# Performance work log

Hardware: AMD Instinct MI355X
Metric: run time of the kernel (lower is better)

## Reference

```python
import jax, jax.numpy as jnp
import numpy as np

B, H, SQ, SKV, D, TOPK = 1, 16, 1024, 4096, 128, 64


def setup_inputs() -> dict:
    key = jax.random.key(0)
    kq, kk, kv, ki, ks = jax.random.split(key, 5)
    q = jax.random.normal(kq, (B, H, SQ, D), dtype=jnp.float32)
    k = jax.random.normal(kk, (B, H, SKV, D), dtype=jnp.float32)
    v = jax.random.normal(kv, (B, H, SKV, D), dtype=jnp.float32)
    topk_indices = jax.random.randint(ki, (B, SQ, TOPK), 0, SKV, dtype=jnp.int32)
    topk_scores = jax.random.uniform(ks, (B, SQ, TOPK), dtype=jnp.float32)
    return {"q": q, "k": k, "v": v, "topk_indices": topk_indices,
            "topk_scores": topk_scores}


def reference(q, k, v, topk_indices, topk_scores):
    # q: (b,h,s,d); k,v: (b,h,S,d) global (cp_world_size=1 all-gather is identity)
    head_dim = q.shape[-1]
    scale = head_dim ** -0.5
    # Gather selected K/V per query without dense (b,h,s,S,d) expansion.
    # idx: (b,1,s,topk,1) broadcast against (b,h,1,S,d) along axis=3.
    idx = topk_indices[:, None, :, :, None]
    k_g = jnp.take_along_axis(k[:, :, None, :, :], idx, axis=3)  # (b,h,s,t,d)
    v_g = jnp.take_along_axis(v[:, :, None, :, :], idx, axis=3)  # (b,h,s,t,d)
    scores = jnp.einsum("bhsd,bhstd->bhst", q, k_g) * scale
    w = jax.nn.softmax(scores, axis=-1)
    # rescale by indexer scores and renormalize
    w = w * topk_scores[:, None, :, :]
    w = w / (jnp.sum(w, axis=-1, keepdims=True) + 1e-12)
    out = jnp.einsum("bhst,bhstd->bhsd", w, v_g)
    return out
```

## Files before the change

kernel.cpp:

```cpp
#include <hip/hip_runtime.h>
#include <hip/hip_fp16.h>

#define NH  16
#define SQL 1024
#define SKV 4096
#define HD  128
#define TK  64

typedef _Float16 h2_t __attribute__((ext_vector_type(2)));
typedef float    f32x4 __attribute__((ext_vector_type(4)));

__device__ __forceinline__ unsigned pkh(float x, float y) {
    return (unsigned)__half_as_ushort(__float2half(x)) |
           ((unsigned)__half_as_ushort(__float2half(y)) << 16);
}

__global__ __launch_bounds__(256) void cvt_f16(
    const float* __restrict__ k, const float* __restrict__ v,
    unsigned short* __restrict__ kh, unsigned short* __restrict__ vh)
{
    int b = blockIdx.x;
    const float* src; unsigned short* dst;
    if (b < 4096) { src = k; dst = kh; }
    else          { src = v; dst = vh; b -= 4096; }
    const size_t i = (size_t)b * 256 + threadIdx.x;
    const float4* s4 = (const float4*)src;
    float4 a = s4[2 * i], c = s4[2 * i + 1];
    uint4 o;
    o.x = pkh(a.x, a.y);
    o.y = pkh(a.z, a.w);
    o.z = pkh(c.x, c.y);
    o.w = pkh(c.z, c.w);
    ((uint4*)dst)[i] = o;
}

__global__ __launch_bounds__(256, 2) void dsa_phased(
    const float* __restrict__ q, const unsigned short* __restrict__ kh,
    const unsigned short* __restrict__ vh, const int* __restrict__ tidx,
    const float* __restrict__ tsc, float* __restrict__ out)
{
    __shared__ float scr[4][TK][17];

    const int tid  = threadIdx.x;
    const int wv   = tid >> 6;
    const int lane = tid & 63;
    const int quad = lane >> 4;
    const int l16  = lane & 15;
    const int bi   = blockIdx.x;
    const int xcd  = bi & 7;
    const int tile = bi >> 3;
    const int sb   = tile * 16 + wv * 4;

    int   tIdx[4];
    float tSc[4];
#pragma unroll
    for (int qi = 0; qi < 4; ++qi) {
        tIdx[qi] = tidx[(sb + qi) * TK + lane];
        tSc[qi]  = tsc[(sb + qi) * TK + lane];
    }

    for (int rnd = 0; rnd < 2; ++rnd) {
        const int h = xcd | (rnd << 3);
        const unsigned short* kb = kh + (size_t)h * SKV * HD;
        const unsigned short* vb = vh + (size_t)h * SKV * HD;
        unsigned wpk[4];

#pragma unroll
        for (int qi = 0; qi < 4; ++qi) {
            const int s = sb + qi;
            const float* qp = q + (size_t)(h * SQL + s) * HD + 8 * l16;
            const f32x4 qa = __builtin_nontemporal_load((const f32x4*)qp);
            const f32x4 qb = __builtin_nontemporal_load((const f32x4*)qp + 1);
            h2_t q0 = {(_Float16)qa.x, (_Float16)qa.y};
            h2_t q1 = {(_Float16)qa.z, (_Float16)qa.w};
            h2_t q2 = {(_Float16)qb.x, (_Float16)qb.y};
            h2_t q3 = {(_Float16)qb.z, (_Float16)qb.w};

            float part[16];
#pragma unroll
            for (int i = 0; i < 16; ++i) {
                const size_t row = (size_t)__shfl(tIdx[qi], 4 * i + quad);
                uint4 kw = *(const uint4*)(kb + row * HD + 8 * l16);
                float d = 0.f;
#if __has_builtin(__builtin_amdgcn_fdot2)
                d = __builtin_amdgcn_fdot2(q0, __builtin_bit_cast(h2_t, kw.x), d, false);
                d = __builtin_amdgcn_fdot2(q1, __builtin_bit_cast(h2_t, kw.y), d, false);
                d = __builtin_amdgcn_fdot2(q2, __builtin_bit_cast(h2_t, kw.z), d, false);
                d = __builtin_amdgcn_fdot2(q3, __builtin_bit_cast(h2_t, kw.w), d, false);
#else
                {
                    float2 k0 = __half22float2(__builtin_bit_cast(__half2, kw.x));
                    float2 k1 = __half22float2(__builtin_bit_cast(__half2, kw.y));
                    float2 k2 = __half22float2(__builtin_bit_cast(__half2, kw.z));
                    float2 k3 = __half22float2(__builtin_bit_cast(__half2, kw.w));
                    d  = qa.x * k0.x + qa.y * k0.y + qa.z * k1.x + qa.w * k1.y;
                    d += qb.x * k2.x + qb.y * k2.y + qb.z * k3.x + qb.w * k3.y;
                }
#endif
                part[i] = d;
            }

#pragma unroll
            for (int i = 0; i < 16; ++i) scr[wv][4 * i + quad][l16] = part[i];
            float acc = 0.f;
#pragma unroll
            for (int m = 0; m < 16; ++m) acc += scr[wv][lane][m];
            acc *= 0.08838834764831845f;

            float mx = acc;
#pragma unroll
            for (int off = 32; off; off >>= 1) mx = fmaxf(mx, __shfl_xor(mx, off));
            const float e   = __expf(acc - mx);
            const float ets = e * tSc[qi];
            float se = e, sets = ets;
#pragma unroll
            for (int off = 32; off; off >>= 1) {
                se   += __shfl_xor(se, off);
                sets += __shfl_xor(sets, off);
            }
            const float w = ets / (sets + 1e-12f * se);
            wpk[qi] = __builtin_bit_cast(unsigned, __float2half2_rn(w));
        }

        __syncthreads();

#pragma unroll
        for (int qi = 0; qi < 4; ++qi) {
            const int s = sb + qi;
            __half2 o0 = __float2half2_rn(0.f);
            __half2 o1 = o0, o2 = o0, o3 = o0;
#pragma unroll
            for (int i = 0; i < 16; ++i) {
                const size_t row = (size_t)__shfl(tIdx[qi], 4 * i + quad);
                uint4 vw = *(const uint4*)(vb + row * HD + 8 * l16);
                const __half2 w2 =
                    __builtin_bit_cast(__half2, __shfl(wpk[qi], 4 * i + quad));
                o0 = __hfma2(w2, __builtin_bit_cast(__half2, vw.x), o0);
                o1 = __hfma2(w2, __builtin_bit_cast(__half2, vw.y), o1);
                o2 = __hfma2(w2, __builtin_bit_cast(__half2, vw.z), o2);
                o3 = __hfma2(w2, __builtin_bit_cast(__half2, vw.w), o3);
            }

            __half2 oo[4] = {o0, o1, o2, o3};
#pragma unroll
            for (int j = 0; j < 4; ++j) {
                unsigned u = __builtin_bit_cast(unsigned, oo[j]);
                oo[j] = __hadd2(oo[j], __builtin_bit_cast(__half2, __shfl_xor(u, 16)));
                u = __builtin_bit_cast(unsigned, oo[j]);
                oo[j] = __hadd2(oo[j], __builtin_bit_cast(__half2, __shfl_xor(u, 32)));
            }

            if (quad == 0) {
                float2 f0 = __half22float2(oo[0]);
                float2 f1 = __half22float2(oo[1]);
                float2 f2 = __half22float2(oo[2]);
                float2 f3 = __half22float2(oo[3]);
                float* op = out + (size_t)(h * SQL + s) * HD + 8 * l16;
                f32x4 w0 = {f0.x, f0.y, f1.x, f1.y};
                f32x4 w1 = {f2.x, f2.y, f3.x, f3.y};
                __builtin_nontemporal_store(w0, (f32x4*)op);
                __builtin_nontemporal_store(w1, (f32x4*)op + 1);
            }
        }
        if (rnd == 0) __syncthreads();
    }
}

__global__ __launch_bounds__(256) void dsa_fp32(
    const float* __restrict__ q, const float* __restrict__ k,
    const float* __restrict__ v, const int* __restrict__ tidx,
    const float* __restrict__ tsc, float* __restrict__ out)
{
    __shared__ int   idxs[4][TK];
    __shared__ float wsc[4][TK];
    const int tid = threadIdx.x, wv = tid >> 6, lane = tid & 63;
    const int half = lane >> 5, l32 = lane & 31, bi = blockIdx.x;
    const int h = ((bi & 7) << 1) | ((bi >> 3) & 1);
    const int s = ((bi >> 4) << 2) + wv;
    const float* qp = q + (size_t)(h * SQL + s) * HD;
    const float4 qf = *(const float4*)(qp + 4 * l32);
    const float t_sc = tsc[s * TK + lane];
    idxs[wv][lane] = tidx[s * TK + lane];
    const float* kb = k + (size_t)h * SKV * HD;
#pragma unroll 4
    for (int i = 0; i < TK / 2; ++i) {
        const int t = 2 * i + half, row = idxs[wv][t];
        float4 k4 = *(const float4*)(kb + (size_t)row * HD + 4 * l32);
        float d = k4.x * qf.x + k4.y * qf.y + k4.z * qf.z + k4.w * qf.w;
        d += __shfl_xor(d, 16); d += __shfl_xor(d, 8); d += __shfl_xor(d, 4);
        d += __shfl_xor(d, 2);  d += __shfl_xor(d, 1);
        if (l32 == 0) wsc[wv][t] = d;
    }
    float acc = wsc[wv][lane] * 0.08838834764831845f;
    float m = acc;
#pragma unroll
    for (int off = 32; off; off >>= 1) m = fmaxf(m, __shfl_xor(m, off));
    const float e = __expf(acc - m), ets = e * t_sc;
    float se = e, sets = ets;
#pragma unroll
    for (int off = 32; off; off >>= 1) { se += __shfl_xor(se, off); sets += __shfl_xor(sets, off); }
    wsc[wv][lane] = ets / (sets + 1e-12f * se);
    const float* vbp = v + (size_t)h * SKV * HD;
    float4 o = make_float4(0.f, 0.f, 0.f, 0.f);
#pragma unroll 4
    for (int i = 0; i < TK / 2; ++i) {
        const int t = 2 * i + half, row = idxs[wv][t];
        const float wt = wsc[wv][t];
        float4 v4 = *(const float4*)(vbp + (size_t)row * HD + 4 * l32);
        o.x += wt * v4.x; o.y += wt * v4.y; o.z += wt * v4.z; o.w += wt * v4.w;
    }
    o.x += __shfl_xor(o.x, 32); o.y += __shfl_xor(o.y, 32);
    o.z += __shfl_xor(o.z, 32); o.w += __shfl_xor(o.w, 32);
    if (half == 0) *(float4*)(out + (size_t)(h * SQL + s) * HD + 4 * l32) = o;
}

extern "C" void kernel_launch(void* const* d_in, const int* in_sizes, int n_in,
                              void* d_out, int out_size, void* d_ws, size_t ws_size,
                              hipStream_t stream) {
    const float* q  = (const float*)d_in[0];
    const float* k  = (const float*)d_in[1];
    const float* v  = (const float*)d_in[2];
    const int*   ti = (const int*)d_in[3];
    const float* ts = (const float*)d_in[4];
    float* out = (float*)d_out;

    const size_t nkv  = (size_t)NH * SKV * HD;
    const size_t need = 2 * nkv * sizeof(unsigned short);
    if (ws_size >= need) {
        unsigned short* kh = (unsigned short*)d_ws;
        unsigned short* vh = kh + nkv;
        cvt_f16<<<dim3(8192), dim3(256), 0, stream>>>(k, v, kh, vh);
        dsa_phased<<<dim3(512), dim3(256), 0, stream>>>(q, kh, vh, ti, ts, out);
    } else {
        dsa_fp32<<<dim3(4096), dim3(256), 0, stream>>>(q, k, v, ti, ts, out);
    }
}
```

Baseline: 133.5 us.

## Drop fp16 K/V conversion pass and gather fp32 K/V directly

Removes the separate kernel that converted all of K and V to fp16 in a workspace, and has the attention kernel gather fp32 K/V rows directly, using fp32 FMAs for the dot products and the weighted V sum. The fp16 pass read and wrote all 64 MB of K/V even though the top-64 gather touches only part of it, so skipping it avoids that full-tensor traffic and one kernel launch. Each wave now handles two queries instead of four, and the grid doubles to 1024 blocks to keep the GPU busy. In exchange each gathered row is twice as many bytes, and the fp32 fallback path is deleted.

```diff
diff --git a/kernel.cpp b/kernel.cpp
--- a/kernel.cpp
+++ b/kernel.cpp
@@ -1,5 +1,4 @@
 #include <hip/hip_runtime.h>
-#include <hip/hip_fp16.h>
 
 #define NH  16
 #define SQL 1024
@@ -7,36 +6,11 @@
 #define HD  128
 #define TK  64
 
-typedef _Float16 h2_t __attribute__((ext_vector_type(2)));
-typedef float    f32x4 __attribute__((ext_vector_type(4)));
+typedef float f32x4 __attribute__((ext_vector_type(4)));
 
-__device__ __forceinline__ unsigned pkh(float x, float y) {
-    return (unsigned)__half_as_ushort(__float2half(x)) |
-           ((unsigned)__half_as_ushort(__float2half(y)) << 16);
-}
-
-__global__ __launch_bounds__(256) void cvt_f16(
-    const float* __restrict__ k, const float* __restrict__ v,
-    unsigned short* __restrict__ kh, unsigned short* __restrict__ vh)
-{
-    int b = blockIdx.x;
-    const float* src; unsigned short* dst;
-    if (b < 4096) { src = k; dst = kh; }
-    else          { src = v; dst = vh; b -= 4096; }
-    const size_t i = (size_t)b * 256 + threadIdx.x;
-    const float4* s4 = (const float4*)src;
-    float4 a = s4[2 * i], c = s4[2 * i + 1];
-    uint4 o;
-    o.x = pkh(a.x, a.y);
-    o.y = pkh(a.z, a.w);
-    o.z = pkh(c.x, c.y);
-    o.w = pkh(c.z, c.w);
-    ((uint4*)dst)[i] = o;
-}
-
-__global__ __launch_bounds__(256, 2) void dsa_phased(
-    const float* __restrict__ q, const unsigned short* __restrict__ kh,
-    const unsigned short* __restrict__ vh, const int* __restrict__ tidx,
+__global__ __launch_bounds__(256) void dsa_direct(
+    const float* __restrict__ q, const float* __restrict__ k,
+    const float* __restrict__ v, const int* __restrict__ tidx,
     const float* __restrict__ tsc, float* __restrict__ out)
 {
     __shared__ float scr[4][TK][17];
@@ -49,54 +23,44 @@
     const int bi   = blockIdx.x;
     const int xcd  = bi & 7;
     const int tile = bi >> 3;
-    const int sb   = tile * 16 + wv * 4;
+    const int sb   = tile * 8 + wv * 2;
 
-    int   tIdx[4];
-    float tSc[4];
+    int   tIdx[2];
+    float tSc[2];
 #pragma unroll
-    for (int qi = 0; qi < 4; ++qi) {
+    for (int qi = 0; qi < 2; ++qi) {
         tIdx[qi] = tidx[(sb + qi) * TK + lane];
         tSc[qi]  = tsc[(sb + qi) * TK + lane];
     }
 
     for (int rnd = 0; rnd < 2; ++rnd) {
         const int h = xcd | (rnd << 3);
-        const unsigned short* kb = kh + (size_t)h * SKV * HD;
-        const unsigned short* vb = vh + (size_t)h * SKV * HD;
-        unsigned wpk[4];
+        const float* kb = k + (size_t)h * SKV * HD;
+        const float* vb = v + (size_t)h * SKV * HD;
+        float wq[2];
 
 #pragma unroll
-        for (int qi = 0; qi < 4; ++qi) {
+        for (int qi = 0; qi < 2; ++qi) {
             const int s = sb + qi;
             const float* qp = q + (size_t)(h * SQL + s) * HD + 8 * l16;
             const f32x4 qa = __builtin_nontemporal_load((const f32x4*)qp);
             const f32x4 qb = __builtin_nontemporal_load((const f32x4*)qp + 1);
-            h2_t q0 = {(_Float16)qa.x, (_Float16)qa.y};
-            h2_t q1 = {(_Float16)qa.z, (_Float16)qa.w};
-            h2_t q2 = {(_Float16)qb.x, (_Float16)qb.y};
-            h2_t q3 = {(_Float16)qb.z, (_Float16)qb.w};
 
             float part[16];
 #pragma unroll
             for (int i = 0; i < 16; ++i) {
                 const size_t row = (size_t)__shfl(tIdx[qi], 4 * i + quad);
-                uint4 kw = *(const uint4*)(kb + row * HD + 8 * l16);
-                float d = 0.f;
-#if __has_builtin(__builtin_amdgcn_fdot2)
-                d = __builtin_amdgcn_fdot2(q0, __builtin_bit_cast(h2_t, kw.x), d, false);
-                d = __builtin_amdgcn_fdot2(q1, __builtin_bit_cast(h2_t, kw.y), d, false);
-                d = __builtin_amdgcn_fdot2(q2, __builtin_bit_cast(h2_t, kw.z), d, false);
-                d = __builtin_amdgcn_fdot2(q3, __builtin_bit_cast(h2_t, kw.w), d, false);
-#else
-                {
-                    float2 k0 = __half22float2(__builtin_bit_cast(__half2, kw.x));
-                    float2 k1 = __half22float2(__builtin_bit_cast(__half2, kw.y));
-                    float2 k2 = __half22float2(__builtin_bit_cast(__half2, kw.z));
-                    float2 k3 = __half22float2(__builtin_bit_cast(__half2, kw.w));
-                    d  = qa.x * k0.x + qa.y * k0.y + qa.z * k1.x + qa.w * k1.y;
-                    d += qb.x * k2.x + qb.y * k2.y + qb.z * k3.x + qb.w * k3.y;
-                }
-#endif
+                const f32x4 ka = *(const f32x4*)(kb + row * HD + 8 * l16);
+                const f32x4 kc = *(const f32x4*)(kb + row * HD + 8 * l16 + 4);
+                float d;
+                d = qa.x * ka.x;
+                d = fmaf(qa.y, ka.y, d);
+                d = fmaf(qa.z, ka.z, d);
+                d = fmaf(qa.w, ka.w, d);
+                d = fmaf(qb.x, kc.x, d);
+                d = fmaf(qb.y, kc.y, d);
+                d = fmaf(qb.z, kc.z, d);
+                d = fmaf(qb.w, kc.w, d);
                 part[i] = d;
             }
 
@@ -118,100 +82,49 @@
                 se   += __shfl_xor(se, off);
                 sets += __shfl_xor(sets, off);
             }
-            const float w = ets / (sets + 1e-12f * se);
-            wpk[qi] = __builtin_bit_cast(unsigned, __float2half2_rn(w));
+            wq[qi] = ets / (sets + 1e-12f * se);
         }
 
         __syncthreads();
 
 #pragma unroll
-        for (int qi = 0; qi < 4; ++qi) {
+        for (int qi = 0; qi < 2; ++qi) {
             const int s = sb + qi;
-            __half2 o0 = __float2half2_rn(0.f);
-            __half2 o1 = o0, o2 = o0, o3 = o0;
+            float o0 = 0.f, o1 = 0.f, o2 = 0.f, o3 = 0.f;
+            float o4 = 0.f, o5 = 0.f, o6 = 0.f, o7 = 0.f;
 #pragma unroll
             for (int i = 0; i < 16; ++i) {
                 const size_t row = (size_t)__shfl(tIdx[qi], 4 * i + quad);
-                uint4 vw = *(const uint4*)(vb + row * HD + 8 * l16);
-                const __half2 w2 =
-                    __builtin_bit_cast(__half2, __shfl(wpk[qi], 4 * i + quad));
-                o0 = __hfma2(w2, __builtin_bit_cast(__half2, vw.x), o0);
-                o1 = __hfma2(w2, __builtin_bit_cast(__half2, vw.y), o1);
-                o2 = __hfma2(w2, __builtin_bit_cast(__half2, vw.z), o2);
-                o3 = __hfma2(w2, __builtin_bit_cast(__half2, vw.w), o3);
+                const f32x4 va = *(const f32x4*)(vb + row * HD + 8 * l16);
+                const f32x4 vc = *(const f32x4*)(vb + row * HD + 8 * l16 + 4);
+                const float wt = __shfl(wq[qi], 4 * i + quad);
+                o0 = fmaf(wt, va.x, o0);
+                o1 = fmaf(wt, va.y, o1);
+                o2 = fmaf(wt, va.z, o2);
+                o3 = fmaf(wt, va.w, o3);
+                o4 = fmaf(wt, vc.x, o4);
+                o5 = fmaf(wt, vc.y, o5);
+                o6 = fmaf(wt, vc.z, o6);
+                o7 = fmaf(wt, vc.w, o7);
             }
 
-            __half2 oo[4] = {o0, o1, o2, o3};
+            float oo[8] = {o0, o1, o2, o3, o4, o5, o6, o7};
 #pragma unroll
-            for (int j = 0; j < 4; ++j) {
-                unsigned u = __builtin_bit_cast(unsigned, oo[j]);
-                oo[j] = __hadd2(oo[j], __builtin_bit_cast(__half2, __shfl_xor(u, 16)));
-                u = __builtin_bit_cast(unsigned, oo[j]);
-                oo[j] = __hadd2(oo[j], __builtin_bit_cast(__half2, __shfl_xor(u, 32)));
+            for (int j = 0; j < 8; ++j) {
+                oo[j] += __shfl_xor(oo[j], 16);
+                oo[j] += __shfl_xor(oo[j], 32);
             }
 
             if (quad == 0) {
-                float2 f0 = __half22float2(oo[0]);
-                float2 f1 = __half22float2(oo[1]);
-                float2 f2 = __half22float2(oo[2]);
-                float2 f3 = __half22float2(oo[3]);
                 float* op = out + (size_t)(h * SQL + s) * HD + 8 * l16;
-                f32x4 w0 = {f0.x, f0.y, f1.x, f1.y};
-                f32x4 w1 = {f2.x, f2.y, f3.x, f3.y};
+                f32x4 w0 = {oo[0], oo[1], oo[2], oo[3]};
+                f32x4 w1 = {oo[4], oo[5], oo[6], oo[7]};
                 __builtin_nontemporal_store(w0, (f32x4*)op);
                 __builtin_nontemporal_store(w1, (f32x4*)op + 1);
             }
         }
         if (rnd == 0) __syncthreads();
     }
-}
-
-__global__ __launch_bounds__(256) void dsa_fp32(
-    const float* __restrict__ q, const float* __restrict__ k,
-    const float* __restrict__ v, const int* __restrict__ tidx,
-    const float* __restrict__ tsc, float* __restrict__ out)
-{
-    __shared__ int   idxs[4][TK];
-    __shared__ float wsc[4][TK];
-    const int tid = threadIdx.x, wv = tid >> 6, lane = tid & 63;
-    const int half = lane >> 5, l32 = lane & 31, bi = blockIdx.x;
-    const int h = ((bi & 7) << 1) | ((bi >> 3) & 1);
-    const int s = ((bi >> 4) << 2) + wv;
-    const float* qp = q + (size_t)(h * SQL + s) * HD;
-    const float4 qf = *(const float4*)(qp + 4 * l32);
-    const float t_sc = tsc[s * TK + lane];
-    idxs[wv][lane] = tidx[s * TK + lane];
-    const float* kb = k + (size_t)h * SKV * HD;
-#pragma unroll 4
-    for (int i = 0; i < TK / 2; ++i) {
-        const int t = 2 * i + half, row = idxs[wv][t];
-        float4 k4 = *(const float4*)(kb + (size_t)row * HD + 4 * l32);
-        float d = k4.x * qf.x + k4.y * qf.y + k4.z * qf.z + k4.w * qf.w;
-        d += __shfl_xor(d, 16); d += __shfl_xor(d, 8); d += __shfl_xor(d, 4);
-        d += __shfl_xor(d, 2);  d += __shfl_xor(d, 1);
-        if (l32 == 0) wsc[wv][t] = d;
-    }
-    float acc = wsc[wv][lane] * 0.08838834764831845f;
-    float m = acc;
-#pragma unroll
-    for (int off = 32; off; off >>= 1) m = fmaxf(m, __shfl_xor(m, off));
-    const float e = __expf(acc - m), ets = e * t_sc;
-    float se = e, sets = ets;
-#pragma unroll
-    for (int off = 32; off; off >>= 1) { se += __shfl_xor(se, off); sets += __shfl_xor(sets, off); }
-    wsc[wv][lane] = ets / (sets + 1e-12f * se);
-    const float* vbp = v + (size_t)h * SKV * HD;
-    float4 o = make_float4(0.f, 0.f, 0.f, 0.f);
-#pragma unroll 4
-    for (int i = 0; i < TK / 2; ++i) {
-        const int t = 2 * i + half, row = idxs[wv][t];
-        const float wt = wsc[wv][t];
-        float4 v4 = *(const float4*)(vbp + (size_t)row * HD + 4 * l32);
-        o.x += wt * v4.x; o.y += wt * v4.y; o.z += wt * v4.z; o.w += wt * v4.w;
-    }
-    o.x += __shfl_xor(o.x, 32); o.y += __shfl_xor(o.y, 32);
-    o.z += __shfl_xor(o.z, 32); o.w += __shfl_xor(o.w, 32);
-    if (half == 0) *(float4*)(out + (size_t)(h * SQL + s) * HD + 4 * l32) = o;
 }
 
 extern "C" void kernel_launch(void* const* d_in, const int* in_sizes, int n_in,
@@ -224,14 +137,6 @@
     const float* ts = (const float*)d_in[4];
     float* out = (float*)d_out;
 
-    const size_t nkv  = (size_t)NH * SKV * HD;
-    const size_t need = 2 * nkv * sizeof(unsigned short);
-    if (ws_size >= need) {
-        unsigned short* kh = (unsigned short*)d_ws;
-        unsigned short* vh = kh + nkv;
-        cvt_f16<<<dim3(8192), dim3(256), 0, stream>>>(k, v, kh, vh);
-        dsa_phased<<<dim3(512), dim3(256), 0, stream>>>(q, kh, vh, ti, ts, out);
-    } else {
-        dsa_fp32<<<dim3(4096), dim3(256), 0, stream>>>(q, k, v, ti, ts, out);
-    }
+    (void)d_ws; (void)ws_size;
+    dsa_direct<<<dim3(1024), dim3(256), 0, stream>>>(q, k, v, ti, ts, out);
 }
```

New measurement: 166.3 us. 24.6% more time.

## Align f16 conversion with XCD head mapping and use one query per wave

Applied to the files above, without the earlier changes.

The K/V fp32-to-f16 conversion kernel now assigns blocks so each XCD converts the heads that the same XCD later gathers in the attention kernel, aiming for L2 locality between kernels. The attention kernel is restructured so each wave processes a single query rather than four, quadrupling the grid and reducing per-thread register state. This trades some redundant per-block setup for more parallelism and latency hiding.

```diff
diff --git a/kernel.cpp b/kernel.cpp
--- a/kernel.cpp
+++ b/kernel.cpp
@@ -7,7 +7,7 @@
 #define HD  128
 #define TK  64
 
-typedef _Float16 h2_t __attribute__((ext_vector_type(2)));
+typedef _Float16 h2_t  __attribute__((ext_vector_type(2)));
 typedef float    f32x4 __attribute__((ext_vector_type(4)));
 
 __device__ __forceinline__ unsigned pkh(float x, float y) {
@@ -15,26 +15,37 @@
            ((unsigned)__half_as_ushort(__float2half(y)) << 16);
 }
 
-__global__ __launch_bounds__(256) void cvt_f16(
+__global__ __launch_bounds__(256) void cvt_f16_xcd(
     const float* __restrict__ k, const float* __restrict__ v,
     unsigned short* __restrict__ kh, unsigned short* __restrict__ vh)
 {
-    int b = blockIdx.x;
-    const float* src; unsigned short* dst;
-    if (b < 4096) { src = k; dst = kh; }
-    else          { src = v; dst = vh; b -= 4096; }
-    const size_t i = (size_t)b * 256 + threadIdx.x;
-    const float4* s4 = (const float4*)src;
-    float4 a = s4[2 * i], c = s4[2 * i + 1];
-    uint4 o;
-    o.x = pkh(a.x, a.y);
-    o.y = pkh(a.z, a.w);
-    o.z = pkh(c.x, c.y);
-    o.w = pkh(c.z, c.w);
-    ((uint4*)dst)[i] = o;
-}
-
-__global__ __launch_bounds__(256, 2) void dsa_phased(
+    const int b   = blockIdx.x;
+    const int xcd = b & 7;
+    const int j   = b >> 3;
+    const int isK = j >> 8;
+    const int hsel= (j >> 7) & 1;
+    const int chk = j & 127;
+    const int h   = xcd | (hsel << 3);
+
+    const float*    src = isK ? k  : v;
+    unsigned short* dst = isK ? kh : vh;
+    const size_t base = (size_t)h * SKV * HD + (size_t)chk * 4096
+                      + (size_t)threadIdx.x * 16;
+    const float4* s4 = (const float4*)(src + base);
+    uint4*        d4 = (uint4*)(dst + base);
+#pragma unroll
+    for (int u = 0; u < 2; ++u) {
+        float4 a = s4[2 * u], c = s4[2 * u + 1];
+        uint4 o;
+        o.x = pkh(a.x, a.y);
+        o.y = pkh(a.z, a.w);
+        o.z = pkh(c.x, c.y);
+        o.w = pkh(c.z, c.w);
+        d4[u] = o;
+    }
+}
+
+__global__ __launch_bounds__(256) void dsa_f16p(
     const float* __restrict__ q, const unsigned short* __restrict__ kh,
     const unsigned short* __restrict__ vh, const int* __restrict__ tidx,
     const float* __restrict__ tsc, float* __restrict__ out)
@@ -48,120 +59,105 @@
     const int l16  = lane & 15;
     const int bi   = blockIdx.x;
     const int xcd  = bi & 7;
-    const int tile = bi >> 3;
-    const int sb   = tile * 16 + wv * 4;
-
-    int   tIdx[4];
-    float tSc[4];
-#pragma unroll
-    for (int qi = 0; qi < 4; ++qi) {
-        tIdx[qi] = tidx[(sb + qi) * TK + lane];
-        tSc[qi]  = tsc[(sb + qi) * TK + lane];
-    }
+    const int s0   = (bi >> 3) * 4 + wv;
+
+    const int   tIdx = tidx[s0 * TK + lane];
+    const float tSc  = tsc[s0 * TK + lane];
 
     for (int rnd = 0; rnd < 2; ++rnd) {
         const int h = xcd | (rnd << 3);
         const unsigned short* kb = kh + (size_t)h * SKV * HD;
         const unsigned short* vb = vh + (size_t)h * SKV * HD;
-        unsigned wpk[4];
-
-#pragma unroll
-        for (int qi = 0; qi < 4; ++qi) {
-            const int s = sb + qi;
-            const float* qp = q + (size_t)(h * SQL + s) * HD + 8 * l16;
-            const f32x4 qa = __builtin_nontemporal_load((const f32x4*)qp);
-            const f32x4 qb = __builtin_nontemporal_load((const f32x4*)qp + 1);
-            h2_t q0 = {(_Float16)qa.x, (_Float16)qa.y};
-            h2_t q1 = {(_Float16)qa.z, (_Float16)qa.w};
-            h2_t q2 = {(_Float16)qb.x, (_Float16)qb.y};
-            h2_t q3 = {(_Float16)qb.z, (_Float16)qb.w};
-
-            float part[16];
-#pragma unroll
-            for (int i = 0; i < 16; ++i) {
-                const size_t row = (size_t)__shfl(tIdx[qi], 4 * i + quad);
-                uint4 kw = *(const uint4*)(kb + row * HD + 8 * l16);
-                float d = 0.f;
+
+        const float* qp = q + (size_t)(h * SQL + s0) * HD + 8 * l16;
+        const f32x4 qa = __builtin_nontemporal_load((const f32x4*)qp);
+        const f32x4 qb = __builtin_nontemporal_load((const f32x4*)qp + 1);
+        h2_t q0 = {(_Float16)qa.x, (_Float16)qa.y};
+        h2_t q1 = {(_Float16)qa.z, (_Float16)qa.w};
+        h2_t q2 = {(_Float16)qb.x, (_Float16)qb.y};
+        h2_t q3 = {(_Float16)qb.z, (_Float16)qb.w};
+
+        float part[16];
+#pragma unroll
+        for (int i = 0; i < 16; ++i) {
+            const size_t row = (size_t)__shfl(tIdx, 4 * i + quad);
+            uint4 kw = *(const uint4*)(kb + row * HD + 8 * l16);
+            float d = 0.f;
 #if __has_builtin(__builtin_amdgcn_fdot2)
-                d = __builtin_amdgcn_fdot2(q0, __builtin_bit_cast(h2_t, kw.x), d, false);
-                d = __builtin_amdgcn_fdot2(q1, __builtin_bit_cast(h2_t, kw.y), d, false);
-                d = __builtin_amdgcn_fdot2(q2, __builtin_bit_cast(h2_t, kw.z), d, false);
-                d = __builtin_amdgcn_fdot2(q3, __builtin_bit_cast(h2_t, kw.w), d, false);
+            d = __builtin_amdgcn_fdot2(q0, __builtin_bit_cast(h2_t, kw.x), d, false);
+            d = __builtin_amdgcn_fdot2(q1, __builtin_bit_cast(h2_t, kw.y), d, false);
+            d = __builtin_amdgcn_fdot2(q2, __builtin_bit_cast(h2_t, kw.z), d, false);
+            d = __builtin_amdgcn_fdot2(q3, __builtin_bit_cast(h2_t, kw.w), d, false);
 #else
-                {
-                    float2 k0 = __half22float2(__builtin_bit_cast(__half2, kw.x));
-                    float2 k1 = __half22float2(__builtin_bit_cast(__half2, kw.y));
-                    float2 k2 = __half22float2(__builtin_bit_cast(__half2, kw.z));
-                    float2 k3 = __half22float2(__builtin_bit_cast(__half2, kw.w));
-                    d  = qa.x * k0.x + qa.y * k0.y + qa.z * k1.x + qa.w * k1.y;
-                    d += qb.x * k2.x + qb.y * k2.y + qb.z * k3.x + qb.w * k3.y;
-                }
+            {
+                float2 k0 = __half22float2(__builtin_bit_cast(__half2, kw.x));
+                float2 k1 = __half22float2(__builtin_bit_cast(__half2, kw.y));
+                float2 k2 = __half22float2(__builtin_bit_cast(__half2, kw.z));
+                float2 k3 = __half22float2(__builtin_bit_cast(__half2, kw.w));
+                d  = qa.x * k0.x + qa.y * k0.y + qa.z * k1.x + qa.w * k1.y;
+                d += qb.x * k2.x + qb.y * k2.y + qb.z * k3.x + qb.w * k3.y;
+            }
 #endif
-                part[i] = d;
-            }
-
-#pragma unroll
-            for (int i = 0; i < 16; ++i) scr[wv][4 * i + quad][l16] = part[i];
-            float acc = 0.f;
-#pragma unroll
-            for (int m = 0; m < 16; ++m) acc += scr[wv][lane][m];
-            acc *= 0.08838834764831845f;
-
-            float mx = acc;
-#pragma unroll
-            for (int off = 32; off; off >>= 1) mx = fmaxf(mx, __shfl_xor(mx, off));
-            const float e   = __expf(acc - mx);
-            const float ets = e * tSc[qi];
-            float se = e, sets = ets;
-#pragma unroll
-            for (int off = 32; off; off >>= 1) {
-                se   += __shfl_xor(se, off);
-                sets += __shfl_xor(sets, off);
-            }
-            const float w = ets / (sets + 1e-12f * se);
-            wpk[qi] = __builtin_bit_cast(unsigned, __float2half2_rn(w));
-        }
+            part[i] = d;
+        }
+
+#pragma unroll
+        for (int i = 0; i < 16; ++i) scr[wv][4 * i + quad][l16] = part[i];
+        float acc = 0.f;
+#pragma unroll
+        for (int m = 0; m < 16; ++m) acc += scr[wv][lane][m];
+        acc *= 0.08838834764831845f;
+
+        float mx = acc;
+#pragma unroll
+        for (int off = 32; off; off >>= 1) mx = fmaxf(mx, __shfl_xor(mx, off));
+        const float e   = __expf(acc - mx);
+        const float ets = e * tSc;
+        float se = e, sets = ets;
+#pragma unroll
+        for (int off = 32; off; off >>= 1) {
+            se   += __shfl_xor(se, off);
+            sets += __shfl_xor(sets, off);
+        }
+        const float w = ets / (sets + 1e-12f * se);
+        const unsigned wpk = __builtin_bit_cast(unsigned, __float2half2_rn(w));
 
         __syncthreads();
 
-#pragma unroll
-        for (int qi = 0; qi < 4; ++qi) {
-            const int s = sb + qi;
-            __half2 o0 = __float2half2_rn(0.f);
-            __half2 o1 = o0, o2 = o0, o3 = o0;
-#pragma unroll
-            for (int i = 0; i < 16; ++i) {
-                const size_t row = (size_t)__shfl(tIdx[qi], 4 * i + quad);
-                uint4 vw = *(const uint4*)(vb + row * HD + 8 * l16);
-                const __half2 w2 =
-                    __builtin_bit_cast(__half2, __shfl(wpk[qi], 4 * i + quad));
-                o0 = __hfma2(w2, __builtin_bit_cast(__half2, vw.x), o0);
-                o1 = __hfma2(w2, __builtin_bit_cast(__half2, vw.y), o1);
-                o2 = __hfma2(w2, __builtin_bit_cast(__half2, vw.z), o2);
-                o3 = __hfma2(w2, __builtin_bit_cast(__half2, vw.w), o3);
-            }
-
-            __half2 oo[4] = {o0, o1, o2, o3};
-#pragma unroll
-            for (int j = 0; j < 4; ++j) {
-                unsigned u = __builtin_bit_cast(unsigned, oo[j]);
-                oo[j] = __hadd2(oo[j], __builtin_bit_cast(__half2, __shfl_xor(u, 16)));
-                u = __builtin_bit_cast(unsigned, oo[j]);
-                oo[j] = __hadd2(oo[j], __builtin_bit_cast(__half2, __shfl_xor(u, 32)));
-            }
-
-            if (quad == 0) {
-                float2 f0 = __half22float2(oo[0]);
-                float2 f1 = __half22float2(oo[1]);
-                float2 f2 = __half22float2(oo[2]);
-                float2 f3 = __half22float2(oo[3]);
-                float* op = out + (size_t)(h * SQL + s) * HD + 8 * l16;
-                f32x4 w0 = {f0.x, f0.y, f1.x, f1.y};
-                f32x4 w1 = {f2.x, f2.y, f3.x, f3.y};
-                __builtin_nontemporal_store(w0, (f32x4*)op);
-                __builtin_nontemporal_store(w1, (f32x4*)op + 1);
-            }
-        }
+        __half2 o0 = __float2half2_rn(0.f);
+        __half2 o1 = o0, o2 = o0, o3 = o0;
+#pragma unroll
+        for (int i = 0; i < 16; ++i) {
+            const size_t row = (size_t)__shfl(tIdx, 4 * i + quad);
+            uint4 vw = *(const uint4*)(vb + row * HD + 8 * l16);
+            const __half2 w2 = __builtin_bit_cast(__half2, __shfl(wpk, 4 * i + quad));
+            o0 = __hfma2(w2, __builtin_bit_cast(__half2, vw.x), o0);
+            o1 = __hfma2(w2, __builtin_bit_cast(__half2, vw.y), o1);
+            o2 = __hfma2(w2, __builtin_bit_cast(__half2, vw.z), o2);
+            o3 = __hfma2(w2, __builtin_bit_cast(__half2, vw.w), o3);
+        }
+
+        __half2 oo[4] = {o0, o1, o2, o3};
+#pragma unroll
+        for (int j = 0; j < 4; ++j) {
+            unsigned u = __builtin_bit_cast(unsigned, oo[j]);
+            oo[j] = __hadd2(oo[j], __builtin_bit_cast(__half2, __shfl_xor(u, 16)));
+            u = __builtin_bit_cast(unsigned, oo[j]);
+            oo[j] = __hadd2(oo[j], __builtin_bit_cast(__half2, __shfl_xor(u, 32)));
+        }
+
+        if (quad == 0) {
+            float2 f0 = __half22float2(oo[0]);
+            float2 f1 = __half22float2(oo[1]);
+            float2 f2 = __half22float2(oo[2]);
+            float2 f3 = __half22float2(oo[3]);
+            float* op = out + (size_t)(h * SQL + s0) * HD + 8 * l16;
+            f32x4 w0 = {f0.x, f0.y, f1.x, f1.y};
+            f32x4 w1 = {f2.x, f2.y, f3.x, f3.y};
+            __builtin_nontemporal_store(w0, (f32x4*)op);
+            __builtin_nontemporal_store(w1, (f32x4*)op + 1);
+        }
+
         if (rnd == 0) __syncthreads();
     }
 }
@@ -229,8 +225,8 @@
     if (ws_size >= need) {
         unsigned short* kh = (unsigned short*)d_ws;
         unsigned short* vh = kh + nkv;
-        cvt_f16<<<dim3(8192), dim3(256), 0, stream>>>(k, v, kh, vh);
-        dsa_phased<<<dim3(512), dim3(256), 0, stream>>>(q, kh, vh, ti, ts, out);
+        cvt_f16_xcd<<<dim3(4096), dim3(256), 0, stream>>>(k, v, kh, vh);
+        dsa_f16p<<<dim3(2048), dim3(256), 0, stream>>>(q, kh, vh, ti, ts, out);
     } else {
         dsa_fp32<<<dim3(4096), dim3(256), 0, stream>>>(q, k, v, ti, ts, out);
     }
```

New measurement: 137.2 us. +2.8%, slower.

## Quantize K to per-row int8 with float scales for the score dot products

Applied to the files above, without the earlier changes.

The conversion kernel now quantizes K rows to int8 with a per-row absmax scale, while V stays fp16. The attention kernel reads 8-byte int8 K fragments plus a per-row scale and does the dot product in fp32 FMAs. This halves K gather bytes and the K workspace write, at the cost of more ALU work per element and lower score precision, which may hurt accuracy.

```diff
diff --git a/kernel.cpp b/kernel.cpp
--- a/kernel.cpp
+++ b/kernel.cpp
@@ -7,7 +7,7 @@
 #define HD  128
 #define TK  64
 
-typedef _Float16 h2_t __attribute__((ext_vector_type(2)));
+typedef _Float16 h2_t  __attribute__((ext_vector_type(2)));
 typedef float    f32x4 __attribute__((ext_vector_type(4)));
 
 __device__ __forceinline__ unsigned pkh(float x, float y) {
@@ -15,29 +15,62 @@
            ((unsigned)__half_as_ushort(__float2half(y)) << 16);
 }
 
-__global__ __launch_bounds__(256) void cvt_f16(
+__global__ __launch_bounds__(256) void cvt_mixed(
     const float* __restrict__ k, const float* __restrict__ v,
-    unsigned short* __restrict__ kh, unsigned short* __restrict__ vh)
+    signed char* __restrict__ kq, float* __restrict__ ksc,
+    unsigned short* __restrict__ vh)
 {
     int b = blockIdx.x;
-    const float* src; unsigned short* dst;
-    if (b < 4096) { src = k; dst = kh; }
-    else          { src = v; dst = vh; b -= 4096; }
-    const size_t i = (size_t)b * 256 + threadIdx.x;
-    const float4* s4 = (const float4*)src;
-    float4 a = s4[2 * i], c = s4[2 * i + 1];
-    uint4 o;
-    o.x = pkh(a.x, a.y);
-    o.y = pkh(a.z, a.w);
-    o.z = pkh(c.x, c.y);
-    o.w = pkh(c.z, c.w);
-    ((uint4*)dst)[i] = o;
-}
-
-__global__ __launch_bounds__(256, 2) void dsa_phased(
-    const float* __restrict__ q, const unsigned short* __restrict__ kh,
-    const unsigned short* __restrict__ vh, const int* __restrict__ tidx,
-    const float* __restrict__ tsc, float* __restrict__ out)
+    if (b < 4096) {
+        const int g   = threadIdx.x >> 4;
+        const int l   = threadIdx.x & 15;
+        const int row = b * 16 + g;
+        const float* src = k + (size_t)row * HD + 8 * l;
+        const f32x4 a = __builtin_nontemporal_load((const f32x4*)src);
+        const f32x4 c = __builtin_nontemporal_load((const f32x4*)src + 1);
+
+        float m = fmaxf(fmaxf(fmaxf(fabsf(a.x), fabsf(a.y)),
+                              fmaxf(fabsf(a.z), fabsf(a.w))),
+                        fmaxf(fmaxf(fabsf(c.x), fabsf(c.y)),
+                              fmaxf(fabsf(c.z), fabsf(c.w))));
+        m = fmaxf(m, __shfl_xor(m, 1));
+        m = fmaxf(m, __shfl_xor(m, 2));
+        m = fmaxf(m, __shfl_xor(m, 4));
+        m = fmaxf(m, __shfl_xor(m, 8));
+
+        const float scale  = m * (1.0f / 127.0f);
+        const float rscale = (m > 0.f) ? 127.0f / m : 0.f;
+
+        int q0 = (int)rintf(a.x * rscale), q1 = (int)rintf(a.y * rscale);
+        int q2 = (int)rintf(a.z * rscale), q3 = (int)rintf(a.w * rscale);
+        int q4 = (int)rintf(c.x * rscale), q5 = (int)rintf(c.y * rscale);
+        int q6 = (int)rintf(c.z * rscale), q7 = (int)rintf(c.w * rscale);
+        uint2 o;
+        o.x = (unsigned)(q0 & 0xFF) | ((unsigned)(q1 & 0xFF) << 8) |
+              ((unsigned)(q2 & 0xFF) << 16) | ((unsigned)(q3 & 0xFF) << 24);
+        o.y = (unsigned)(q4 & 0xFF) | ((unsigned)(q5 & 0xFF) << 8) |
+              ((unsigned)(q6 & 0xFF) << 16) | ((unsigned)(q7 & 0xFF) << 24);
+        *(uint2*)(kq + (size_t)row * HD + 8 * l) = o;
+        if (l == 0) ksc[row] = scale;
+    } else {
+        b -= 4096;
+        const size_t i = (size_t)b * 256 + threadIdx.x;
+        const float4* s4 = (const float4*)v;
+        float4 a = s4[2 * i], c = s4[2 * i + 1];
+        uint4 o;
+        o.x = pkh(a.x, a.y);
+        o.y = pkh(a.z, a.w);
+        o.z = pkh(c.x, c.y);
+        o.w = pkh(c.z, c.w);
+        ((uint4*)vh)[i] = o;
+    }
+}
+
+__global__ __launch_bounds__(256, 2) void dsa_k8i(
+    const float* __restrict__ q, const signed char* __restrict__ kq,
+    const float* __restrict__ ksc, const unsigned short* __restrict__ vh,
+    const int* __restrict__ tidx, const float* __restrict__ tsc,
+    float* __restrict__ out)
 {
     __shared__ float scr[4][TK][17];
 
@@ -61,8 +94,9 @@
 
     for (int rnd = 0; rnd < 2; ++rnd) {
         const int h = xcd | (rnd << 3);
-        const unsigned short* kb = kh + (size_t)h * SKV * HD;
-        const unsigned short* vb = vh + (size_t)h * SKV * HD;
+        const signed char*    kb = kq  + (size_t)h * SKV * HD;
+        const float*          ks = ksc + (size_t)h * SKV;
+        const unsigned short* vb = vh  + (size_t)h * SKV * HD;
         unsigned wpk[4];
 
 #pragma unroll
@@ -71,33 +105,24 @@
             const float* qp = q + (size_t)(h * SQL + s) * HD + 8 * l16;
             const f32x4 qa = __builtin_nontemporal_load((const f32x4*)qp);
             const f32x4 qb = __builtin_nontemporal_load((const f32x4*)qp + 1);
-            h2_t q0 = {(_Float16)qa.x, (_Float16)qa.y};
-            h2_t q1 = {(_Float16)qa.z, (_Float16)qa.w};
-            h2_t q2 = {(_Float16)qb.x, (_Float16)qb.y};
-            h2_t q3 = {(_Float16)qb.z, (_Float16)qb.w};
 
             float part[16];
 #pragma unroll
             for (int i = 0; i < 16; ++i) {
                 const size_t row = (size_t)__shfl(tIdx[qi], 4 * i + quad);
-                uint4 kw = *(const uint4*)(kb + row * HD + 8 * l16);
-                float d = 0.f;
-#if __has_builtin(__builtin_amdgcn_fdot2)
-                d = __builtin_amdgcn_fdot2(q0, __builtin_bit_cast(h2_t, kw.x), d, false);
-                d = __builtin_amdgcn_fdot2(q1, __builtin_bit_cast(h2_t, kw.y), d, false);
-                d = __builtin_amdgcn_fdot2(q2, __builtin_bit_cast(h2_t, kw.z), d, false);
-                d = __builtin_amdgcn_fdot2(q3, __builtin_bit_cast(h2_t, kw.w), d, false);
-#else
-                {
-                    float2 k0 = __half22float2(__builtin_bit_cast(__half2, kw.x));
-                    float2 k1 = __half22float2(__builtin_bit_cast(__half2, kw.y));
-                    float2 k2 = __half22float2(__builtin_bit_cast(__half2, kw.z));
-                    float2 k3 = __half22float2(__builtin_bit_cast(__half2, kw.w));
-                    d  = qa.x * k0.x + qa.y * k0.y + qa.z * k1.x + qa.w * k1.y;
-                    d += qb.x * k2.x + qb.y * k2.y + qb.z * k3.x + qb.w * k3.y;
-                }
-#endif
-                part[i] = d;
+                const uint2 kw = *(const uint2*)(kb + row * HD + 8 * l16);
+                const float sc = ks[row];
+                const int w0 = (int)kw.x, w1 = (int)kw.y;
+                float d;
+                d = qa.x * (float)(signed char)(w0);
+                d = fmaf(qa.y, (float)(signed char)(w0 >> 8),  d);
+                d = fmaf(qa.z, (float)(signed char)(w0 >> 16), d);
+                d = fmaf(qa.w, (float)(w0 >> 24),              d);
+                d = fmaf(qb.x, (float)(signed char)(w1),       d);
+                d = fmaf(qb.y, (float)(signed char)(w1 >> 8),  d);
+                d = fmaf(qb.z, (float)(signed char)(w1 >> 16), d);
+                d = fmaf(qb.w, (float)(w1 >> 24),              d);
+                part[i] = d * sc;
             }
 
 #pragma unroll
@@ -224,13 +249,15 @@
     const float* ts = (const float*)d_in[4];
     float* out = (float*)d_out;
 
-    const size_t nkv  = (size_t)NH * SKV * HD;
-    const size_t need = 2 * nkv * sizeof(unsigned short);
+    const size_t nkv   = (size_t)NH * SKV * HD;
+    const size_t scb   = (size_t)NH * SKV * sizeof(float);
+    const size_t need  = nkv + scb + nkv * sizeof(unsigned short);
     if (ws_size >= need) {
-        unsigned short* kh = (unsigned short*)d_ws;
-        unsigned short* vh = kh + nkv;
-        cvt_f16<<<dim3(8192), dim3(256), 0, stream>>>(k, v, kh, vh);
-        dsa_phased<<<dim3(512), dim3(256), 0, stream>>>(q, kh, vh, ti, ts, out);
+        signed char*    kq  = (signed char*)d_ws;
+        float*          ksc = (float*)(kq + nkv);
+        unsigned short* vh  = (unsigned short*)((char*)ksc + scb);
+        cvt_mixed<<<dim3(8192), dim3(256), 0, stream>>>(k, v, kq, ksc, vh);
+        dsa_k8i<<<dim3(512), dim3(256), 0, stream>>>(q, kq, ksc, vh, ti, ts, out);
     } else {
         dsa_fp32<<<dim3(4096), dim3(256), 0, stream>>>(q, k, v, ti, ts, out);
     }
```

After: 162.7 us. +21.8%, slower.
